# Kernel tuning notes

Hardware: AMD Instinct MI355X
Metric: run time of the kernel (lower is better)

The kernel has to match this reference:

```python
import jax, jax.numpy as jnp
import numpy as np

C = 256
H = 4  # hard-coded head count in SA_Layer reshapes
EPS = 1e-5


def _bn(x, gamma, beta):
    # training-mode BatchNorm1d over (batch, length) per channel; x: [b,c,n]
    m = jnp.mean(x, axis=(0, 2), keepdims=True)
    v = jnp.var(x, axis=(0, 2), keepdims=True)
    return gamma[None, :, None] * (x - m) * jax.lax.rsqrt(v + EPS) + beta[None, :, None]


def _conv1(w, x, b=None):
    # 1x1 Conv1d == per-point matmul; w: [o,c], x: [b,c,n]
    y = jnp.einsum('oc,bcn->bon', w, x)
    return y if b is None else y + b[None, :, None]


def _sa_layer(x, xyz_emb, qk_w, v_w, v_b, t_w, t_b, bn_g, bn_b):
    b, c, n = x.shape
    h = x + xyz_emb                      # [b,c,n]
    q = _conv1(qk_w, h)                  # [b,c,n]  (q and k share weights)
    # quirky reshape: permute to [b,n,c] then view as [b,H,n,c//H]
    x_q = jnp.transpose(q, (0, 2, 1)).reshape(b, H, n, c // H)
    x_k = q.reshape(b, H, c // H, n)     # standard channel head split
    x_v = _conv1(v_w, h, v_b).reshape(b, H, c // H, n)
    energy = jnp.matmul(x_q, x_k)        # [b,H,n,n]
    att = jax.nn.softmax(energy, axis=-1)
    att = jax.nn.softmax(att, axis=-2)   # dual softmax
    x_r = jnp.matmul(x_v, att).reshape(b, c, n)
    x_r = jax.nn.relu(_bn(_conv1(t_w, x - x_r, t_b), bn_g, bn_b))
    return x + x_r


def setup_inputs() -> dict:
    key = jax.random.key(0)
    ks = jax.random.split(key, 16)
    B, N = 4, 2048
    s = 1.0 / np.sqrt(C)
    inp = {
        'x': jax.random.normal(ks[0], (B, C, N), jnp.float32),
        'xyz': jax.random.normal(ks[1], (B, N, 3), jnp.float32),
        'conv1_w': jax.random.normal(ks[2], (C, C), jnp.float32) * s,
        'pos_w': jax.random.normal(ks[3], (C, 3), jnp.float32) * 0.5,
        'pos_b': jax.random.normal(ks[4], (C,), jnp.float32) * 0.02,
        'bn1_g': jnp.ones((C,), jnp.float32),
        'bn1_b': jnp.zeros((C,), jnp.float32),
        'qk_w': jax.random.normal(ks[5], (4, C, C), jnp.float32) * s,
        'v_w': jax.random.normal(ks[6], (4, C, C), jnp.float32) * s,
        'v_b': jax.random.normal(ks[7], (4, C), jnp.float32) * 0.02,
        't_w': jax.random.normal(ks[8], (4, C, C), jnp.float32) * s,
        't_b': jax.random.normal(ks[9], (4, C), jnp.float32) * 0.02,
        'bn_g': jnp.ones((4, C), jnp.float32),
        'bn_b': jnp.zeros((4, C), jnp.float32),
    }
    return inp


def reference(x, xyz, conv1_w, pos_w, pos_b, bn1_g, bn1_b,
              qk_w, v_w, v_b, t_w, t_b, bn_g, bn_b):
    # xyz: [B,N,3] -> permute -> pos_xyz (1x1 conv)
    xyz_emb = jnp.einsum('oi,bni->bon', pos_w, xyz) + pos_b[None, :, None]  # [b,C,n]
    h = jax.nn.relu(_bn(_conv1(conv1_w, x), bn1_g, bn1_b))
    outs = []
    for i in range(4):
        h = _sa_layer(h, xyz_emb, qk_w[i], v_w[i], v_b[i],
                      t_w[i], t_b[i], bn_g[i], bn_b[i])
        outs.append(h)
    return jnp.concatenate(outs, axis=1)  # [b, 4*C, n]
```

## Files before the change

### kernel.cpp

```cpp
#include <hip/hip_runtime.h>
#include <math.h>

#define Bsz 4
#define Cch 256
#define Npt 2048
#define Hh  4
#define NL  4
#define BN_CNT (Bsz * Npt)
#define EPSV 1e-5f
#define NROW (16 * Npt)
#define L2E 1.44269504f

typedef _Float16 f16x8 __attribute__((ext_vector_type(8)));
typedef _Float16 f16x4 __attribute__((ext_vector_type(4)));
typedef float    f32x4 __attribute__((ext_vector_type(4)));

__device__ __forceinline__ float fexp2(float x) { return __builtin_amdgcn_exp2f(x); }

__device__ __forceinline__ void gld16(const _Float16* g, _Float16* l) {
    __builtin_amdgcn_global_load_lds(
        (const __attribute__((address_space(1))) unsigned int*)g,
        (__attribute__((address_space(3))) unsigned int*)l, 16, 0, 0);
}

__global__ void k_xyz_emb(const float* __restrict__ xyz, const float* __restrict__ pw,
                          const float* __restrict__ pb, float* __restrict__ emb) {
    int idx = blockIdx.x * 256 + threadIdx.x;
    int n = idx & (Npt - 1);
    int c = (idx >> 11) & (Cch - 1);
    int b = idx >> 19;
    const float* xz = xyz + (b * Npt + n) * 3;
    emb[idx] = pw[c * 3 + 0] * xz[0] + pw[c * 3 + 1] * xz[1] + pw[c * 3 + 2] * xz[2] + pb[c];
}

__global__ void k_castw(const float* __restrict__ c1w, const float* __restrict__ qkw,
                        const float* __restrict__ vw, const float* __restrict__ tw,
                        _Float16* __restrict__ o, float* __restrict__ bnacc) {
    int i = blockIdx.x * 256 + threadIdx.x;
    if (i < 5 * 512) bnacc[i] = 0.f;
    const float* src; int off;
    if (i < 65536)            { src = c1w; off = i; }
    else if (i < 327680)      { src = qkw; off = i - 65536; }
    else if (i < 589824)      { src = vw;  off = i - 327680; }
    else                      { src = tw;  off = i - 589824; }
    o[i] = (_Float16)src[off];
}

__global__ __launch_bounds__(256) void k_fuse_t(const float* __restrict__ in,
        _Float16* __restrict__ XT) {
    __shared__ _Float16 Tt[64][72];
    const int b = blockIdx.z, c0 = blockIdx.y * 64, n0 = blockIdx.x * 64;
    const int t = threadIdx.x;
    const int cl = t >> 2, ns = (t & 3) * 16;
    const float* ip = in + ((size_t)(b * Cch + c0 + cl) * Npt) + n0 + ns;
    #pragma unroll
    for (int g = 0; g < 4; ++g) {
        float4 v = *(const float4*)(ip + g * 4);
        Tt[ns + g * 4 + 0][cl] = (_Float16)v.x;
        Tt[ns + g * 4 + 1][cl] = (_Float16)v.y;
        Tt[ns + g * 4 + 2][cl] = (_Float16)v.z;
        Tt[ns + g * 4 + 3][cl] = (_Float16)v.w;
    }
    __syncthreads();
    int nl = t >> 2, cs = (t & 3) * 16;
    _Float16* op = XT + ((size_t)(b * Npt + n0 + nl) * Cch) + c0 + cs;
    #pragma unroll
    for (int g = 0; g < 4; ++g)
        *(f16x4*)(op + g * 4) = *(f16x4*)&Tt[nl][cs + g * 4];
}

__global__ __launch_bounds__(256) void k_gemm_mfma(const _Float16* __restrict__ Wb,
        const _Float16* __restrict__ XT, const float* __restrict__ bias,
        float* __restrict__ Yf, float* __restrict__ bnacc) {
    __shared__ float EpF[64][68];
    const int b = blockIdx.z, o0 = blockIdx.y * 64, n0 = blockIdx.x * 64;
    const int tid = threadIdx.x, w = tid >> 6, quad = (tid >> 4) & 3, tx = tid & 15;
    const _Float16* Arow = Wb + (o0 + w * 16 + tx) * Cch + quad * 8;
    const _Float16* Brow = XT + ((size_t)(b * Npt + n0 + tx) * Cch) + quad * 8;
    f32x4 acc[4];
    #pragma unroll
    for (int s = 0; s < 4; ++s) acc[s] = (f32x4){0.f, 0.f, 0.f, 0.f};
    for (int k0 = 0; k0 < Cch; k0 += 32) {
        f16x8 a = *(const f16x8*)(Arow + k0);
        #pragma unroll
        for (int s = 0; s < 4; ++s) {
            f16x8 bb = *(const f16x8*)(Brow + s * 16 * Cch + k0);
            acc[s] = __builtin_amdgcn_mfma_f32_16x16x32_f16(a, bb, acc[s], 0, 0, 0);
        }
    }
    float bv[4];
    {
        int ob = o0 + w * 16 + quad * 4;
        if (bias) { bv[0] = bias[ob]; bv[1] = bias[ob + 1]; bv[2] = bias[ob + 2]; bv[3] = bias[ob + 3]; }
        else bv[0] = bv[1] = bv[2] = bv[3] = 0.f;
    }
    #pragma unroll
    for (int s = 0; s < 4; ++s) {
        int ol = w * 16 + quad * 4, nl = s * 16 + tx;
        EpF[ol + 0][nl] = acc[s][0] + bv[0];
        EpF[ol + 1][nl] = acc[s][1] + bv[1];
        EpF[ol + 2][nl] = acc[s][2] + bv[2];
        EpF[ol + 3][nl] = acc[s][3] + bv[3];
    }
    __syncthreads();
    int row = tid >> 2, seg = (tid & 3) * 16;
    float* yp = Yf + ((size_t)(b * Cch + o0 + row) * Npt) + n0 + seg;
    float s1 = 0.f, s2 = 0.f;
    #pragma unroll
    for (int g = 0; g < 4; ++g) {
        float4 v = *(float4*)&EpF[row][seg + g * 4];
        *(float4*)(yp + g * 4) = v;
        s1 += v.x + v.y + v.z + v.w;
        s2 += v.x * v.x + v.y * v.y + v.z * v.z + v.w * v.w;
    }
    s1 += __shfl_xor(s1, 1); s2 += __shfl_xor(s2, 1);
    s1 += __shfl_xor(s1, 2); s2 += __shfl_xor(s2, 2);
    if ((tid & 3) == 0) {
        atomicAdd(&bnacc[o0 + row], s1);
        atomicAdd(&bnacc[256 + o0 + row], s2);
    }
}

__global__ __launch_bounds__(256) void k_gemm_qkv(const _Float16* __restrict__ Wqk,
        const _Float16* __restrict__ Wv, const _Float16* __restrict__ XT,
        const float* __restrict__ vbias, _Float16* __restrict__ Vb,
        _Float16* __restrict__ Qg, _Float16* __restrict__ Kt) {
    __shared__ _Float16 EpB[64][72];
    const int b = blockIdx.z, y = blockIdx.y, n0 = blockIdx.x * 64;
    const int isV = (y >= 4);
    const int o0 = (isV ? (y - 4) : y) * 64;
    const _Float16* Wb = isV ? Wv : Wqk;
    const int tid = threadIdx.x, w = tid >> 6, quad = (tid >> 4) & 3, tx = tid & 15;
    const _Float16* Arow = Wb + (o0 + w * 16 + tx) * Cch + quad * 8;
    const _Float16* Brow = XT + ((size_t)(b * Npt + n0 + tx) * Cch) + quad * 8;
    f32x4 acc[4];
    #pragma unroll
    for (int s = 0; s < 4; ++s) acc[s] = (f32x4){0.f, 0.f, 0.f, 0.f};
    for (int k0 = 0; k0 < Cch; k0 += 32) {
        f16x8 a = *(const f16x8*)(Arow + k0);
        #pragma unroll
        for (int s = 0; s < 4; ++s) {
            f16x8 bb = *(const f16x8*)(Brow + s * 16 * Cch + k0);
            acc[s] = __builtin_amdgcn_mfma_f32_16x16x32_f16(a, bb, acc[s], 0, 0, 0);
        }
    }
    if (!isV) {
        const int cch = (w << 1) + (quad >> 1);
        const int hof = (quad & 1) * 4;
        #pragma unroll
        for (int s = 0; s < 4; ++s) {
            int ng = n0 + s * 16 + tx;
            f16x4 pk;
            pk[0] = (_Float16)acc[s][0]; pk[1] = (_Float16)acc[s][1];
            pk[2] = (_Float16)acc[s][2]; pk[3] = (_Float16)acc[s][3];
            int rK = ng & 63, jt = ng >> 6;
            size_t ka = ((size_t)((b * Hh + (o0 >> 6)) * 32 + jt) << 12)
                      + rK * 64 + ((cch ^ (rK & 7)) * 8) + hof;
            *(f16x4*)&Kt[ka] = pk;
            int iQ = ((ng & 511) << 2) + (o0 >> 6);
            int rQ = iQ & 63, it = iQ >> 6;
            size_t qa = ((size_t)((b * Hh + (ng >> 9)) * 32 + it) << 12)
                      + rQ * 64 + ((cch ^ (rQ & 7)) * 8) + hof;
            *(f16x4*)&Qg[qa] = pk;
        }
        return;
    }
    float bv[4];
    {
        int ob = o0 + w * 16 + quad * 4;
        bv[0] = vbias[ob]; bv[1] = vbias[ob + 1]; bv[2] = vbias[ob + 2]; bv[3] = vbias[ob + 3];
    }
    #pragma unroll
    for (int s = 0; s < 4; ++s) {
        int ol = w * 16 + quad * 4, nl = s * 16 + tx;
        EpB[ol + 0][nl] = (_Float16)(acc[s][0] + bv[0]);
        EpB[ol + 1][nl] = (_Float16)(acc[s][1] + bv[1]);
        EpB[ol + 2][nl] = (_Float16)(acc[s][2] + bv[2]);
        EpB[ol + 3][nl] = (_Float16)(acc[s][3] + bv[3]);
    }
    __syncthreads();
    int row = tid >> 2, seg = (tid & 3) * 16;
    _Float16* yp = Vb + ((size_t)(b * Cch + o0 + row) * Npt) + n0 + seg;
    #pragma unroll
    for (int g = 0; g < 4; ++g)
        *(f16x4*)(yp + g * 4) = *(f16x4*)&EpB[row][seg + g * 4];
}

__global__ __launch_bounds__(256) void k_attn_A(const _Float16* __restrict__ Qg,
        const _Float16* __restrict__ Kt, float* __restrict__ mP, float* __restrict__ lP) {
    __shared__ _Float16 Ksh[2][4096];
    const int flat = blockIdx.x;
    const int bh = (flat & 7) * 2 + ((flat >> 3) & 1);
    const int rest = flat >> 4;
    const int i0 = (rest & 15) * 128;
    const int jc = rest >> 4;
    const int tid = threadIdx.x, w = tid >> 6, q = (tid >> 4) & 3, tx = tid & 15;
    const int lane = tid & 63;
    const int sx = tx & 7;
    f16x8 qa[2][2];
    #pragma unroll
    for (int g = 0; g < 2; ++g) {
        const _Float16* Qtile = Qg + ((size_t)(bh * 32 + ((i0 + g * 64) >> 6)) << 12);
        int r = w * 16 + tx;
        qa[g][0] = *(const f16x8*)(Qtile + r * 64 + (q ^ sx) * 8);
        qa[g][1] = *(const f16x8*)(Qtile + r * 64 + ((q + 4) ^ sx) * 8);
    }
    const _Float16* Kbase = Kt + ((size_t)(bh * 32) << 12);
    const int jt0 = jc * 8;
    {
        const _Float16* g = Kbase + ((size_t)jt0 << 12) + (w * 2) * 512 + lane * 8;
        gld16(g,       &Ksh[0][(w * 2 + 0) * 512]);
        gld16(g + 512, &Ksh[0][(w * 2 + 1) * 512]);
    }
    __syncthreads();
    float m2[2][4], l[2][4];
    #pragma unroll
    for (int g = 0; g < 2; ++g)
        #pragma unroll
        for (int r = 0; r < 4; ++r) { m2[g][r] = -1e30f; l[g][r] = 0.f; }
    for (int t = 0; t < 8; ++t) {
        if (t < 7) {
            const _Float16* g = Kbase + ((size_t)(jt0 + t + 1) << 12) + (w * 2) * 512 + lane * 8;
            gld16(g,       &Ksh[(t + 1) & 1][(w * 2 + 0) * 512]);
            gld16(g + 512, &Ksh[(t + 1) & 1][(w * 2 + 1) * 512]);
        }
        const _Float16* kbuf = Ksh[t & 1];
        f32x4 e[2][4];
        #pragma unroll
        for (int s = 0; s < 4; ++s) {
            int r = s * 16 + tx;
            f16x8 kb0 = *(const f16x8*)(kbuf + r * 64 + (q ^ sx) * 8);
            f16x8 kb1 = *(const f16x8*)(kbuf + r * 64 + ((q + 4) ^ sx) * 8);
            #pragma unroll
            for (int g = 0; g < 2; ++g) {
                f32x4 z = (f32x4){0.f, 0.f, 0.f, 0.f};
                z = __builtin_amdgcn_mfma_f32_16x16x32_f16(qa[g][0], kb0, z, 0, 0, 0);
                e[g][s] = __builtin_amdgcn_mfma_f32_16x16x32_f16(qa[g][1], kb1, z, 0, 0, 0);
            }
        }
        #pragma unroll
        for (int g = 0; g < 2; ++g)
            #pragma unroll
            for (int r = 0; r < 4; ++r) {
                float e0 = e[g][0][r] * L2E, e1 = e[g][1][r] * L2E;
                float e2 = e[g][2][r] * L2E, e3 = e[g][3][r] * L2E;
                float lm = fmaxf(fmaxf(e0, e1), fmaxf(e2, e3));
                float nm = fmaxf(m2[g][r], lm);
                l[g][r] = l[g][r] * fexp2(m2[g][r] - nm)
                        + fexp2(e0 - nm) + fexp2(e1 - nm) + fexp2(e2 - nm) + fexp2(e3 - nm);
                m2[g][r] = nm;
            }
        __syncthreads();
    }
    #pragma unroll
    for (int g = 0; g < 2; ++g)
        #pragma unroll
        for (int r = 0; r < 4; ++r) {
            float mm = m2[g][r], ll = l[g][r];
            #pragma unroll
            for (int off = 1; off < 16; off <<= 1) {
                float om = __shfl_xor(mm, off), ol = __shfl_xor(ll, off);
                float nm = fmaxf(mm, om);
                ll = ll * fexp2(mm - nm) + ol * fexp2(om - nm);
                mm = nm;
            }
            if (tx == 0) {
                int idx = bh * Npt + i0 + g * 64 + w * 16 + q * 4 + r;
                mP[jc * NROW + idx] = mm;
                lP[jc * NROW + idx] = ll;
            }
        }
}

__global__ __launch_bounds__(256) void k_attn_B(const _Float16* __restrict__ Qg,
        const _Float16* __restrict__ Kt, const _Float16* __restrict__ Vb,
        const float* __restrict__ mP, const float* __restrict__ lP,
        const float* __restrict__ h, _Float16* __restrict__ XT) {
    __shared__ _Float16 AtT[4][4096];
    __shared__ float mlm[Npt];
    __shared__ float mll[Npt];
    __shared__ float Ssh[4][64];
    __shared__ float rsv[64];
    __shared__ _Float16 Tt[64][72];
    const int flat = blockIdx.x;
    const int bh = (flat & 7) * 2 + ((flat >> 3) & 1);
    const int j0 = (flat >> 4) * 64;
    const int b = bh >> 2, hd = bh & 3;
    const int tid = threadIdx.x, w = tid >> 6, q = (tid >> 4) & 3, tx = tid & 15;
    const int sx = tx & 7;
    {
        const int ib = tid * 8;
        #pragma unroll
        for (int e = 0; e < 2; ++e) {
            int ii = ib + e * 4;
            int idx = bh * Npt + ii;
            float4 m0 = *(const float4*)&mP[idx];
            float4 m1 = *(const float4*)&mP[NROW + idx];
            float4 m2 = *(const float4*)&mP[2 * NROW + idx];
            float4 m3 = *(const float4*)&mP[3 * NROW + idx];
            float4 l0 = *(const float4*)&lP[idx];
            float4 l1 = *(const float4*)&lP[NROW + idx];
            float4 l2 = *(const float4*)&lP[2 * NROW + idx];
            float4 l3 = *(const float4*)&lP[3 * NROW + idx];
            #pragma unroll
            for (int k = 0; k < 4; ++k) {
                float a0 = ((const float*)&m0)[k], a1 = ((const float*)&m1)[k];
                float a2 = ((const float*)&m2)[k], a3 = ((const float*)&m3)[k];
                float mm = fmaxf(fmaxf(a0, a1), fmaxf(a2, a3));
                float ll = ((const float*)&l0)[k] * fexp2(a0 - mm)
                         + ((const float*)&l1)[k] * fexp2(a1 - mm)
                         + ((const float*)&l2)[k] * fexp2(a2 - mm)
                         + ((const float*)&l3)[k] * fexp2(a3 - mm);
                mlm[ii + k] = mm;
                mll[ii + k] = L2E / ll;
            }
        }
    }
    __syncthreads();
    f16x8 kb[4][2];
    const _Float16* Ktile = Kt + ((size_t)(bh * 32 + (j0 >> 6)) << 12);
    #pragma unroll
    for (int nt = 0; nt < 4; ++nt) {
        int r = nt * 16 + tx;
        kb[nt][0] = *(const f16x8*)(Ktile + r * 64 + (q ^ sx) * 8);
        kb[nt][1] = *(const f16x8*)(Ktile + r * 64 + ((q + 4) ^ sx) * 8);
    }
    f32x4 Tacc[4][4];
    #pragma unroll
    for (int mt = 0; mt < 4; ++mt)
        #pragma unroll
        for (int nt = 0; nt < 4; ++nt) Tacc[mt][nt] = (f32x4){0.f, 0.f, 0.f, 0.f};
    float scS[4] = {0.f, 0.f, 0.f, 0.f};
    _Float16* myAt = AtT[w];
    const _Float16* vbase = Vb + (size_t)(b * Cch + hd * 64) * Npt;
    for (int it = 0; it < 8; ++it) {
        const int i0 = w * 512 + it * 64;
        const _Float16* Qtile = Qg + ((size_t)(bh * 32 + (i0 >> 6)) << 12);
        #pragma unroll
        for (int mt = 0; mt < 4; ++mt) {
            int r = mt * 16 + tx;
            f16x8 qa0 = *(const f16x8*)(Qtile + r * 64 + (q ^ sx) * 8);
            f16x8 qa1 = *(const f16x8*)(Qtile + r * 64 + ((q + 4) ^ sx) * 8);
            float4 m2v = *(const float4*)&mlm[i0 + mt * 16 + q * 4];
            float4 liv = *(const float4*)&mll[i0 + mt * 16 + q * 4];
            #pragma unroll
            for (int nt = 0; nt < 4; ++nt) {
                f32x4 z = (f32x4){0.f, 0.f, 0.f, 0.f};
                z = __builtin_amdgcn_mfma_f32_16x16x32_f16(qa0, kb[nt][0], z, 0, 0, 0);
                z = __builtin_amdgcn_mfma_f32_16x16x32_f16(qa1, kb[nt][1], z, 0, 0, 0);
                float a0 = fexp2(fexp2(__builtin_fmaf(z[0], L2E, -m2v.x)) * liv.x);
                float a1 = fexp2(fexp2(__builtin_fmaf(z[1], L2E, -m2v.y)) * liv.y);
                float a2 = fexp2(fexp2(__builtin_fmaf(z[2], L2E, -m2v.z)) * liv.z);
                float a3 = fexp2(fexp2(__builtin_fmaf(z[3], L2E, -m2v.w)) * liv.w);
                scS[nt] += a0 + a1 + a2 + a3;
                f16x4 pk;
                pk[0] = (_Float16)a0; pk[1] = (_Float16)a1;
                pk[2] = (_Float16)a2; pk[3] = (_Float16)a3;
                *(f16x4*)&myAt[(nt * 16 + tx) * 64 + ((2 * mt + (q >> 1)) ^ sx) * 8 + (q & 1) * 4] = pk;
            }
        }
        f16x8 pb[4][2], va[4][2];
        #pragma unroll
        for (int nt = 0; nt < 4; ++nt) {
            int r = nt * 16 + tx;
            pb[nt][0] = *(const f16x8*)&myAt[r * 64 + (q ^ sx) * 8];
            pb[nt][1] = *(const f16x8*)&myAt[r * 64 + ((q + 4) ^ sx) * 8];
        }
        #pragma unroll
        for (int mt = 0; mt < 4; ++mt) {
            const _Float16* vp = vbase + (size_t)(mt * 16 + tx) * Npt + i0 + q * 8;
            va[mt][0] = *(const f16x8*)(vp);
            va[mt][1] = *(const f16x8*)(vp + 32);
        }
        #pragma unroll
        for (int mt = 0; mt < 4; ++mt)
            #pragma unroll
            for (int nt = 0; nt < 4; ++nt) {
                Tacc[mt][nt] = __builtin_amdgcn_mfma_f32_16x16x32_f16(va[mt][0], pb[nt][0], Tacc[mt][nt], 0, 0, 0);
                Tacc[mt][nt] = __builtin_amdgcn_mfma_f32_16x16x32_f16(va[mt][1], pb[nt][1], Tacc[mt][nt], 0, 0, 0);
            }
    }
    #pragma unroll
    for (int mt = 0; mt < 4; ++mt)
        #pragma unroll
        for (int nt = 0; nt < 4; ++nt) {
            f16x4 pk;
            pk[0] = (_Float16)Tacc[mt][nt][0];
            pk[1] = (_Float16)Tacc[mt][nt][1];
            pk[2] = (_Float16)Tacc[mt][nt][2];
            pk[3] = (_Float16)Tacc[mt][nt][3];
            *(f16x4*)&myAt[(nt * 16 + tx) * 64 + mt * 16 + q * 4] = pk;
        }
    #pragma unroll
    for (int nt = 0; nt < 4; ++nt) {
        float s = scS[nt];
        s += __shfl_xor(s, 16);
        s += __shfl_xor(s, 32);
        if (q == 0) Ssh[w][nt * 16 + tx] = s;
    }
    __syncthreads();
    if (tid < 64)
        rsv[tid] = 1.f / (Ssh[0][tid] + Ssh[1][tid] + Ssh[2][tid] + Ssh[3][tid]);
    __syncthreads();
    {
        const int cl = tid >> 2, ns = (tid & 3) * 16;
        const float* hp = h + ((size_t)(b * Cch + hd * 64 + cl) * Npt) + j0 + ns;
        #pragma unroll
        for (int g = 0; g < 4; ++g) {
            float4 hv = *(const float4*)(hp + g * 4);
            #pragma unroll
            for (int k = 0; k < 4; ++k) {
                int jl = ns + g * 4 + k;
                float tv = (float)AtT[0][jl * 64 + cl] + (float)AtT[1][jl * 64 + cl]
                         + (float)AtT[2][jl * 64 + cl] + (float)AtT[3][jl * 64 + cl];
                float hvk = ((const float*)&hv)[k];
                Tt[jl][cl] = (_Float16)(hvk - tv * rsv[jl]);
            }
        }
    }
    __syncthreads();
    {
        int nl = tid >> 2, cs = (tid & 3) * 16;
        _Float16* op = XT + ((size_t)(b * Npt + j0 + nl) * Cch) + hd * 64 + cs;
        #pragma unroll
        for (int g = 0; g < 4; ++g)
            *(f16x4*)(op + g * 4) = *(f16x4*)&Tt[nl][cs + g * 4];
    }
}

__global__ __launch_bounds__(256) void k_bn_fuse(const float* __restrict__ t,
        const float* __restrict__ bnacc,
        const float* __restrict__ g, const float* __restrict__ bt,
        const float* __restrict__ emb, const float* __restrict__ resid,
        float* __restrict__ hout, float* __restrict__ out, _Float16* __restrict__ XT,
        int layer) {
    __shared__ _Float16 Tt[64][72];
    const int b = blockIdx.z, c0 = blockIdx.y * 64, n0 = blockIdx.x * 64;
    const int tt = threadIdx.x;
    const int cl = tt >> 2, ns = (tt & 3) * 16;
    const int c = c0 + cl;
    const float mn = bnacc[c] * (1.f / BN_CNT);
    const float var = bnacc[256 + c] * (1.f / BN_CNT) - mn * mn;
    const float is = rsqrtf(var + EPSV);
    const float gg = g[c], bb = bt[c];
    const size_t rowoff = ((size_t)(b * Cch + c) * Npt) + n0 + ns;
    const float* tp = t + rowoff;
    const float* ep = emb + rowoff;
    const float* rp = resid ? resid + rowoff : nullptr;
    float* hp = hout + rowoff;
    float* op = out ? out + (size_t)b * (NL * Cch * Npt) + (size_t)(layer * Cch + c) * Npt + n0 + ns
                    : nullptr;
    #pragma unroll
    for (int gi = 0; gi < 4; ++gi) {
        float4 v = *(const float4*)(tp + gi * 4);
        float4 y;
        y.x = fmaxf(gg * (v.x - mn) * is + bb, 0.f);
        y.y = fmaxf(gg * (v.y - mn) * is + bb, 0.f);
        y.z = fmaxf(gg * (v.z - mn) * is + bb, 0.f);
        y.w = fmaxf(gg * (v.w - mn) * is + bb, 0.f);
        if (rp) {
            float4 r = *(const float4*)(rp + gi * 4);
            y.x += r.x; y.y += r.y; y.z += r.z; y.w += r.w;
        }
        *(float4*)(hp + gi * 4) = y;
        if (op) *(float4*)(op + gi * 4) = y;
        float4 e = *(const float4*)(ep + gi * 4);
        Tt[ns + gi * 4 + 0][cl] = (_Float16)(y.x + e.x);
        Tt[ns + gi * 4 + 1][cl] = (_Float16)(y.y + e.y);
        Tt[ns + gi * 4 + 2][cl] = (_Float16)(y.z + e.z);
        Tt[ns + gi * 4 + 3][cl] = (_Float16)(y.w + e.w);
    }
    __syncthreads();
    int nl = tt >> 2, cs = (tt & 3) * 16;
    _Float16* xp = XT + ((size_t)(b * Npt + n0 + nl) * Cch) + c0 + cs;
    #pragma unroll
    for (int gi = 0; gi < 4; ++gi)
        *(f16x4*)(xp + gi * 4) = *(f16x4*)&Tt[nl][cs + gi * 4];
}

extern "C" void kernel_launch(void* const* d_in, const int* in_sizes, int n_in,
                              void* d_out, int out_size, void* d_ws, size_t ws_size,
                              hipStream_t stream) {
    (void)in_sizes; (void)n_in; (void)out_size; (void)ws_size;
    const float* x    = (const float*)d_in[0];
    const float* xyz  = (const float*)d_in[1];
    const float* c1w  = (const float*)d_in[2];
    const float* posw = (const float*)d_in[3];
    const float* posb = (const float*)d_in[4];
    const float* bn1g = (const float*)d_in[5];
    const float* bn1b = (const float*)d_in[6];
    const float* qkw  = (const float*)d_in[7];
    const float* vw   = (const float*)d_in[8];
    const float* vb   = (const float*)d_in[9];
    const float* tw   = (const float*)d_in[10];
    const float* tb   = (const float*)d_in[11];
    const float* bng  = (const float*)d_in[12];
    const float* bnb  = (const float*)d_in[13];
    float* out = (float*)d_out;

    const size_t NE = (size_t)Bsz * Cch * Npt;
    char* W = (char*)d_ws;
    float* emb   = (float*)W;                 W += NE * 4;
    float* h     = (float*)W;                 W += NE * 4;
    float* vbuf  = (float*)W;                 W += NE * 4;
    _Float16* XT = (_Float16*)W;              W += NE * 2;
    _Float16* Qg = (_Float16*)W;              W += NE * 2;
    _Float16* Kt = (_Float16*)W;              W += NE * 2;
    _Float16* Vb = (_Float16*)W;              W += NE * 2;
    _Float16* wbf = (_Float16*)W;             W += 851968 * 2;
    float* mP    = (float*)W;                 W += 4 * NROW * 4;
    float* lP    = (float*)W;                 W += 4 * NROW * 4;
    float* bnacc = (float*)W;                 W += 5 * 512 * 4;

    dim3 blk(256);
    dim3 g4(Npt / 64, Cch / 64, Bsz);
    dim3 gQKV(Npt / 64, 8, Bsz);
    int ew = (int)(NE / 256);

    k_castw<<<3328, blk, 0, stream>>>(c1w, qkw, vw, tw, wbf, bnacc);
    k_xyz_emb<<<ew, blk, 0, stream>>>(xyz, posw, posb, emb);

    k_fuse_t<<<g4, blk, 0, stream>>>(x, XT);
    k_gemm_mfma<<<g4, blk, 0, stream>>>(wbf, XT, nullptr, vbuf, bnacc);
    k_bn_fuse<<<g4, blk, 0, stream>>>(vbuf, bnacc, bn1g, bn1b, emb, nullptr,
                                      h, nullptr, XT, 0);

    for (int L = 0; L < NL; ++L) {
        const _Float16* qkL = wbf + 65536 + (size_t)L * 65536;
        const _Float16* vL  = wbf + 327680 + (size_t)L * 65536;
        const _Float16* tL  = wbf + 589824 + (size_t)L * 65536;
        float* accL = bnacc + (1 + L) * 512;
        k_gemm_qkv<<<gQKV, blk, 0, stream>>>(qkL, vL, XT, vb + L * Cch, Vb, Qg, Kt);
        k_attn_A<<<1024, blk, 0, stream>>>(Qg, Kt, mP, lP);
        k_attn_B<<<512, blk, 0, stream>>>(Qg, Kt, Vb, mP, lP, h, XT);
        k_gemm_mfma<<<g4, blk, 0, stream>>>(tL, XT, tb + L * Cch, vbuf, accL);
        k_bn_fuse<<<g4, blk, 0, stream>>>(vbuf, accL, bng + L * Cch, bnb + L * Cch,
                                          emb, h, h, out, XT, L);
    }
}
```

Measured before the change: 603.4 us.

## Halve attn_B column tile to 32 and double grid, rewrite epilogue

Shrinks each k_attn_B block from 64 to 32 output columns (j), doubling the grid from 512 to 1024 blocks and halving per-block LDS and accumulator registers. The aim is better occupancy and more parallelism across CUs. The cost is that every block recomputes the full Q·K exponentials over all 2048 rows and reloads V for only half as many columns, which doubles that redundant work. The epilogue now writes the transposed accumulator with a swizzled layout and reads it back directly, with no separate Tt staging buffer or extra barrier.

```diff
diff --git a/kernel.cpp b/kernel.cpp
--- a/kernel.cpp
+++ b/kernel.cpp
@@ -276,15 +276,14 @@
         const _Float16* __restrict__ Kt, const _Float16* __restrict__ Vb,
         const float* __restrict__ mP, const float* __restrict__ lP,
         const float* __restrict__ h, _Float16* __restrict__ XT) {
-    __shared__ _Float16 AtT[4][4096];
+    __shared__ _Float16 AtT[4][2048];
     __shared__ float mlm[Npt];
     __shared__ float mll[Npt];
-    __shared__ float Ssh[4][64];
-    __shared__ float rsv[64];
-    __shared__ _Float16 Tt[64][72];
+    __shared__ float Ssh[4][32];
+    __shared__ float rsv[32];
     const int flat = blockIdx.x;
     const int bh = (flat & 7) * 2 + ((flat >> 3) & 1);
-    const int j0 = (flat >> 4) * 64;
+    const int j0 = (flat >> 4) * 32;
     const int b = bh >> 2, hd = bh & 3;
     const int tid = threadIdx.x, w = tid >> 6, q = (tid >> 4) & 3, tx = tid & 15;
     const int sx = tx & 7;
@@ -317,20 +316,21 @@
         }
     }
     __syncthreads();
-    f16x8 kb[4][2];
+    f16x8 kb[2][2];
     const _Float16* Ktile = Kt + ((size_t)(bh * 32 + (j0 >> 6)) << 12);
-    #pragma unroll
-    for (int nt = 0; nt < 4; ++nt) {
-        int r = nt * 16 + tx;
+    const int jb = j0 & 32;
+    #pragma unroll
+    for (int nt = 0; nt < 2; ++nt) {
+        int r = jb + nt * 16 + tx;
         kb[nt][0] = *(const f16x8*)(Ktile + r * 64 + (q ^ sx) * 8);
         kb[nt][1] = *(const f16x8*)(Ktile + r * 64 + ((q + 4) ^ sx) * 8);
     }
-    f32x4 Tacc[4][4];
+    f32x4 Tacc[4][2];
     #pragma unroll
     for (int mt = 0; mt < 4; ++mt)
         #pragma unroll
-        for (int nt = 0; nt < 4; ++nt) Tacc[mt][nt] = (f32x4){0.f, 0.f, 0.f, 0.f};
-    float scS[4] = {0.f, 0.f, 0.f, 0.f};
+        for (int nt = 0; nt < 2; ++nt) Tacc[mt][nt] = (f32x4){0.f, 0.f, 0.f, 0.f};
+    float scS[2] = {0.f, 0.f};
     _Float16* myAt = AtT[w];
     const _Float16* vbase = Vb + (size_t)(b * Cch + hd * 64) * Npt;
     for (int it = 0; it < 8; ++it) {
@@ -344,7 +344,7 @@
             float4 m2v = *(const float4*)&mlm[i0 + mt * 16 + q * 4];
             float4 liv = *(const float4*)&mll[i0 + mt * 16 + q * 4];
             #pragma unroll
-            for (int nt = 0; nt < 4; ++nt) {
+            for (int nt = 0; nt < 2; ++nt) {
                 f32x4 z = (f32x4){0.f, 0.f, 0.f, 0.f};
                 z = __builtin_amdgcn_mfma_f32_16x16x32_f16(qa0, kb[nt][0], z, 0, 0, 0);
                 z = __builtin_amdgcn_mfma_f32_16x16x32_f16(qa1, kb[nt][1], z, 0, 0, 0);
@@ -359,9 +359,9 @@
                 *(f16x4*)&myAt[(nt * 16 + tx) * 64 + ((2 * mt + (q >> 1)) ^ sx) * 8 + (q & 1) * 4] = pk;
             }
         }
-        f16x8 pb[4][2], va[4][2];
-        #pragma unroll
-        for (int nt = 0; nt < 4; ++nt) {
+        f16x8 pb[2][2], va[4][2];
+        #pragma unroll
+        for (int nt = 0; nt < 2; ++nt) {
             int r = nt * 16 + tx;
             pb[nt][0] = *(const f16x8*)&myAt[r * 64 + (q ^ sx) * 8];
             pb[nt][1] = *(const f16x8*)&myAt[r * 64 + ((q + 4) ^ sx) * 8];
@@ -375,7 +375,7 @@
         #pragma unroll
         for (int mt = 0; mt < 4; ++mt)
             #pragma unroll
-            for (int nt = 0; nt < 4; ++nt) {
+            for (int nt = 0; nt < 2; ++nt) {
                 Tacc[mt][nt] = __builtin_amdgcn_mfma_f32_16x16x32_f16(va[mt][0], pb[nt][0], Tacc[mt][nt], 0, 0, 0);
                 Tacc[mt][nt] = __builtin_amdgcn_mfma_f32_16x16x32_f16(va[mt][1], pb[nt][1], Tacc[mt][nt], 0, 0, 0);
             }
@@ -383,48 +383,42 @@
     #pragma unroll
     for (int mt = 0; mt < 4; ++mt)
         #pragma unroll
-        for (int nt = 0; nt < 4; ++nt) {
+        for (int nt = 0; nt < 2; ++nt) {
             f16x4 pk;
             pk[0] = (_Float16)Tacc[mt][nt][0];
             pk[1] = (_Float16)Tacc[mt][nt][1];
             pk[2] = (_Float16)Tacc[mt][nt][2];
             pk[3] = (_Float16)Tacc[mt][nt][3];
-            *(f16x4*)&myAt[(nt * 16 + tx) * 64 + mt * 16 + q * 4] = pk;
-        }
-    #pragma unroll
-    for (int nt = 0; nt < 4; ++nt) {
+            *(f16x4*)&myAt[(nt * 16 + tx) * 64 + ((2 * mt + (q >> 1)) ^ sx) * 8 + (q & 1) * 4] = pk;
+        }
+    #pragma unroll
+    for (int nt = 0; nt < 2; ++nt) {
         float s = scS[nt];
         s += __shfl_xor(s, 16);
         s += __shfl_xor(s, 32);
         if (q == 0) Ssh[w][nt * 16 + tx] = s;
     }
     __syncthreads();
-    if (tid < 64)
+    if (tid < 32)
         rsv[tid] = 1.f / (Ssh[0][tid] + Ssh[1][tid] + Ssh[2][tid] + Ssh[3][tid]);
     __syncthreads();
     {
-        const int cl = tid >> 2, ns = (tid & 3) * 16;
-        const float* hp = h + ((size_t)(b * Cch + hd * 64 + cl) * Npt) + j0 + ns;
-        #pragma unroll
-        for (int g = 0; g < 4; ++g) {
-            float4 hv = *(const float4*)(hp + g * 4);
-            #pragma unroll
-            for (int k = 0; k < 4; ++k) {
-                int jl = ns + g * 4 + k;
-                float tv = (float)AtT[0][jl * 64 + cl] + (float)AtT[1][jl * 64 + cl]
-                         + (float)AtT[2][jl * 64 + cl] + (float)AtT[3][jl * 64 + cl];
-                float hvk = ((const float*)&hv)[k];
-                Tt[jl][cl] = (_Float16)(hvk - tv * rsv[jl]);
-            }
-        }
-    }
-    __syncthreads();
-    {
-        int nl = tid >> 2, cs = (tid & 3) * 16;
-        _Float16* op = XT + ((size_t)(b * Npt + j0 + nl) * Cch) + hd * 64 + cs;
-        #pragma unroll
-        for (int g = 0; g < 4; ++g)
-            *(f16x4*)(op + g * 4) = *(f16x4*)&Tt[nl][cs + g * 4];
+        const int jl = tid >> 3, half = tid & 7;
+        const int slot = ((half ^ (jl & 7)) * 8);
+        const int base = jl * 64 + slot;
+        f16x8 t0 = *(const f16x8*)&AtT[0][base];
+        f16x8 t1 = *(const f16x8*)&AtT[1][base];
+        f16x8 t2 = *(const f16x8*)&AtT[2][base];
+        f16x8 t3 = *(const f16x8*)&AtT[3][base];
+        const float rs = rsv[jl];
+        const float* hp = h + ((size_t)(b * Cch + hd * 64 + half * 8) * Npt) + j0 + jl;
+        f16x8 u;
+        #pragma unroll
+        for (int e = 0; e < 8; ++e) {
+            float tv = (float)t0[e] + (float)t1[e] + (float)t2[e] + (float)t3[e];
+            u[e] = (_Float16)(hp[(size_t)e * Npt] - tv * rs);
+        }
+        *(f16x8*)(XT + ((size_t)(b * Npt + j0 + jl) * Cch) + hd * 64 + half * 8) = u;
     }
 }
 
@@ -532,7 +526,7 @@
         float* accL = bnacc + (1 + L) * 512;
         k_gemm_qkv<<<gQKV, blk, 0, stream>>>(qkL, vL, XT, vb + L * Cch, Vb, Qg, Kt);
         k_attn_A<<<1024, blk, 0, stream>>>(Qg, Kt, mP, lP);
-        k_attn_B<<<512, blk, 0, stream>>>(Qg, Kt, Vb, mP, lP, h, XT);
+        k_attn_B<<<1024, blk, 0, stream>>>(Qg, Kt, Vb, mP, lP, h, XT);
         k_gemm_mfma<<<g4, blk, 0, stream>>>(tL, XT, tb + L * Cch, vbuf, accL);
         k_bn_fuse<<<g4, blk, 0, stream>>>(vbuf, accL, bng + L * Cch, bnb + L * Cch,
                                           emb, h, h, out, XT, L);
```

After: 634.2 us. 5.1% more time.

## Restructure attention-B to 512 threads, register-resident P tiles and permuted V layout

Applied to the files above, without the earlier changes.

The second attention kernel now runs with 8 waves per block, each covering 256 query rows instead of 512. K is staged into LDS with a direct global-to-LDS load instead of being held in registers. The softmax probabilities are passed straight from the QK MFMA outputs into the PV MFMA as register operands, which removes the per-wave LDS round-trip. To make that work, the V store in the QKV GEMM permutes its column layout so V matches the interleaved P fragment order. The cross-wave reduction of the PV partials is done in two halves to fit LDS, trading extra barriers and shared memory for more parallelism and less LDS traffic.

```diff
diff --git a/kernel.cpp b/kernel.cpp
--- a/kernel.cpp
+++ b/kernel.cpp
@@ -180,10 +180,12 @@
     }
     __syncthreads();
     int row = tid >> 2, seg = (tid & 3) * 16;
-    _Float16* yp = Vb + ((size_t)(b * Cch + o0 + row) * Npt) + n0 + seg;
+    const int m = tid & 3;
+    const int pbase = (m >> 1) * 32 + (m & 1) * 4;
+    _Float16* yp = Vb + ((size_t)(b * Cch + o0 + row) * Npt) + n0 + pbase;
     #pragma unroll
     for (int g = 0; g < 4; ++g)
-        *(f16x4*)(yp + g * 4) = *(f16x4*)&EpB[row][seg + g * 4];
+        *(f16x4*)(yp + g * 8) = *(f16x4*)&EpB[row][seg + g * 4];
 }
 
 __global__ __launch_bounds__(256) void k_attn_A(const _Float16* __restrict__ Qg,
@@ -272,125 +274,99 @@
         }
 }
 
-__global__ __launch_bounds__(256) void k_attn_B(const _Float16* __restrict__ Qg,
+__global__ __launch_bounds__(512, 4) void k_attn_B(const _Float16* __restrict__ Qg,
         const _Float16* __restrict__ Kt, const _Float16* __restrict__ Vb,
         const float* __restrict__ mP, const float* __restrict__ lP,
         const float* __restrict__ h, _Float16* __restrict__ XT) {
-    __shared__ _Float16 AtT[4][4096];
+    __shared__ _Float16 Ksh[4096];
     __shared__ float mlm[Npt];
     __shared__ float mll[Npt];
-    __shared__ float Ssh[4][64];
+    __shared__ float Ssh[8][64];
     __shared__ float rsv[64];
-    __shared__ _Float16 Tt[64][72];
+    __shared__ _Float16 TS[8][2048];
     const int flat = blockIdx.x;
     const int bh = (flat & 7) * 2 + ((flat >> 3) & 1);
     const int j0 = (flat >> 4) * 64;
     const int b = bh >> 2, hd = bh & 3;
     const int tid = threadIdx.x, w = tid >> 6, q = (tid >> 4) & 3, tx = tid & 15;
-    const int sx = tx & 7;
+    const int lane = tid & 63, sx = tx & 7;
     {
-        const int ib = tid * 8;
-        #pragma unroll
-        for (int e = 0; e < 2; ++e) {
-            int ii = ib + e * 4;
-            int idx = bh * Npt + ii;
-            float4 m0 = *(const float4*)&mP[idx];
-            float4 m1 = *(const float4*)&mP[NROW + idx];
-            float4 m2 = *(const float4*)&mP[2 * NROW + idx];
-            float4 m3 = *(const float4*)&mP[3 * NROW + idx];
-            float4 l0 = *(const float4*)&lP[idx];
-            float4 l1 = *(const float4*)&lP[NROW + idx];
-            float4 l2 = *(const float4*)&lP[2 * NROW + idx];
-            float4 l3 = *(const float4*)&lP[3 * NROW + idx];
-            #pragma unroll
-            for (int k = 0; k < 4; ++k) {
-                float a0 = ((const float*)&m0)[k], a1 = ((const float*)&m1)[k];
-                float a2 = ((const float*)&m2)[k], a3 = ((const float*)&m3)[k];
-                float mm = fmaxf(fmaxf(a0, a1), fmaxf(a2, a3));
-                float ll = ((const float*)&l0)[k] * fexp2(a0 - mm)
-                         + ((const float*)&l1)[k] * fexp2(a1 - mm)
-                         + ((const float*)&l2)[k] * fexp2(a2 - mm)
-                         + ((const float*)&l3)[k] * fexp2(a3 - mm);
-                mlm[ii + k] = mm;
-                mll[ii + k] = L2E / ll;
-            }
-        }
-    }
-    __syncthreads();
-    f16x8 kb[4][2];
-    const _Float16* Ktile = Kt + ((size_t)(bh * 32 + (j0 >> 6)) << 12);
-    #pragma unroll
-    for (int nt = 0; nt < 4; ++nt) {
-        int r = nt * 16 + tx;
-        kb[nt][0] = *(const f16x8*)(Ktile + r * 64 + (q ^ sx) * 8);
-        kb[nt][1] = *(const f16x8*)(Ktile + r * 64 + ((q + 4) ^ sx) * 8);
-    }
+        const int ii = tid * 4;
+        const int idx = bh * Npt + ii;
+        float4 m0 = *(const float4*)&mP[idx];
+        float4 m1 = *(const float4*)&mP[NROW + idx];
+        float4 m2 = *(const float4*)&mP[2 * NROW + idx];
+        float4 m3 = *(const float4*)&mP[3 * NROW + idx];
+        float4 l0 = *(const float4*)&lP[idx];
+        float4 l1 = *(const float4*)&lP[NROW + idx];
+        float4 l2 = *(const float4*)&lP[2 * NROW + idx];
+        float4 l3 = *(const float4*)&lP[3 * NROW + idx];
+        #pragma unroll
+        for (int k = 0; k < 4; ++k) {
+            float a0 = ((const float*)&m0)[k], a1 = ((const float*)&m1)[k];
+            float a2 = ((const float*)&m2)[k], a3 = ((const float*)&m3)[k];
+            float mm = fmaxf(fmaxf(a0, a1), fmaxf(a2, a3));
+            float ll = ((const float*)&l0)[k] * fexp2(a0 - mm)
+                     + ((const float*)&l1)[k] * fexp2(a1 - mm)
+                     + ((const float*)&l2)[k] * fexp2(a2 - mm)
+                     + ((const float*)&l3)[k] * fexp2(a3 - mm);
+            mlm[ii + k] = mm;
+            mll[ii + k] = L2E / ll;
+        }
+    }
+    gld16(Kt + (((size_t)(bh * 32 + (j0 >> 6))) << 12) + w * 512 + lane * 8, &Ksh[w * 512]);
+    __syncthreads();
     f32x4 Tacc[4][4];
     #pragma unroll
     for (int mt = 0; mt < 4; ++mt)
         #pragma unroll
         for (int nt = 0; nt < 4; ++nt) Tacc[mt][nt] = (f32x4){0.f, 0.f, 0.f, 0.f};
     float scS[4] = {0.f, 0.f, 0.f, 0.f};
-    _Float16* myAt = AtT[w];
     const _Float16* vbase = Vb + (size_t)(b * Cch + hd * 64) * Npt;
-    for (int it = 0; it < 8; ++it) {
-        const int i0 = w * 512 + it * 64;
+    for (int it = 0; it < 4; ++it) {
+        const int i0 = w * 256 + it * 64;
         const _Float16* Qtile = Qg + ((size_t)(bh * 32 + (i0 >> 6)) << 12);
         #pragma unroll
-        for (int mt = 0; mt < 4; ++mt) {
-            int r = mt * 16 + tx;
-            f16x8 qa0 = *(const f16x8*)(Qtile + r * 64 + (q ^ sx) * 8);
-            f16x8 qa1 = *(const f16x8*)(Qtile + r * 64 + ((q + 4) ^ sx) * 8);
-            float4 m2v = *(const float4*)&mlm[i0 + mt * 16 + q * 4];
-            float4 liv = *(const float4*)&mll[i0 + mt * 16 + q * 4];
-            #pragma unroll
-            for (int nt = 0; nt < 4; ++nt) {
-                f32x4 z = (f32x4){0.f, 0.f, 0.f, 0.f};
-                z = __builtin_amdgcn_mfma_f32_16x16x32_f16(qa0, kb[nt][0], z, 0, 0, 0);
-                z = __builtin_amdgcn_mfma_f32_16x16x32_f16(qa1, kb[nt][1], z, 0, 0, 0);
-                float a0 = fexp2(fexp2(__builtin_fmaf(z[0], L2E, -m2v.x)) * liv.x);
-                float a1 = fexp2(fexp2(__builtin_fmaf(z[1], L2E, -m2v.y)) * liv.y);
-                float a2 = fexp2(fexp2(__builtin_fmaf(z[2], L2E, -m2v.z)) * liv.z);
-                float a3 = fexp2(fexp2(__builtin_fmaf(z[3], L2E, -m2v.w)) * liv.w);
-                scS[nt] += a0 + a1 + a2 + a3;
-                f16x4 pk;
-                pk[0] = (_Float16)a0; pk[1] = (_Float16)a1;
-                pk[2] = (_Float16)a2; pk[3] = (_Float16)a3;
-                *(f16x4*)&myAt[(nt * 16 + tx) * 64 + ((2 * mt + (q >> 1)) ^ sx) * 8 + (q & 1) * 4] = pk;
+        for (int pp = 0; pp < 2; ++pp) {
+            f16x4 pk[2][4];
+            #pragma unroll
+            for (int mt2 = 0; mt2 < 2; ++mt2) {
+                const int mt = pp * 2 + mt2;
+                const int r = mt * 16 + tx;
+                f16x8 qa0 = *(const f16x8*)(Qtile + r * 64 + (q ^ sx) * 8);
+                f16x8 qa1 = *(const f16x8*)(Qtile + r * 64 + ((q + 4) ^ sx) * 8);
+                float4 m2v = *(const float4*)&mlm[i0 + mt * 16 + q * 4];
+                float4 liv = *(const float4*)&mll[i0 + mt * 16 + q * 4];
+                #pragma unroll
+                for (int nt = 0; nt < 4; ++nt) {
+                    const int rk = nt * 16 + tx;
+                    f16x8 kb0 = *(const f16x8*)&Ksh[rk * 64 + (q ^ sx) * 8];
+                    f16x8 kb1 = *(const f16x8*)&Ksh[rk * 64 + ((q + 4) ^ sx) * 8];
+                    f32x4 z = (f32x4){0.f, 0.f, 0.f, 0.f};
+                    z = __builtin_amdgcn_mfma_f32_16x16x32_f16(qa0, kb0, z, 0, 0, 0);
+                    z = __builtin_amdgcn_mfma_f32_16x16x32_f16(qa1, kb1, z, 0, 0, 0);
+                    float a0 = fexp2(fexp2(__builtin_fmaf(z[0], L2E, -m2v.x)) * liv.x);
+                    float a1 = fexp2(fexp2(__builtin_fmaf(z[1], L2E, -m2v.y)) * liv.y);
+                    float a2 = fexp2(fexp2(__builtin_fmaf(z[2], L2E, -m2v.z)) * liv.z);
+                    float a3 = fexp2(fexp2(__builtin_fmaf(z[3], L2E, -m2v.w)) * liv.w);
+                    scS[nt] += a0 + a1 + a2 + a3;
+                    f16x4 pkk;
+                    pkk[0] = (_Float16)a0; pkk[1] = (_Float16)a1;
+                    pkk[2] = (_Float16)a2; pkk[3] = (_Float16)a3;
+                    pk[mt2][nt] = pkk;
+                }
             }
-        }
-        f16x8 pb[4][2], va[4][2];
-        #pragma unroll
-        for (int nt = 0; nt < 4; ++nt) {
-            int r = nt * 16 + tx;
-            pb[nt][0] = *(const f16x8*)&myAt[r * 64 + (q ^ sx) * 8];
-            pb[nt][1] = *(const f16x8*)&myAt[r * 64 + ((q + 4) ^ sx) * 8];
-        }
-        #pragma unroll
-        for (int mt = 0; mt < 4; ++mt) {
-            const _Float16* vp = vbase + (size_t)(mt * 16 + tx) * Npt + i0 + q * 8;
-            va[mt][0] = *(const f16x8*)(vp);
-            va[mt][1] = *(const f16x8*)(vp + 32);
-        }
-        #pragma unroll
-        for (int mt = 0; mt < 4; ++mt)
-            #pragma unroll
-            for (int nt = 0; nt < 4; ++nt) {
-                Tacc[mt][nt] = __builtin_amdgcn_mfma_f32_16x16x32_f16(va[mt][0], pb[nt][0], Tacc[mt][nt], 0, 0, 0);
-                Tacc[mt][nt] = __builtin_amdgcn_mfma_f32_16x16x32_f16(va[mt][1], pb[nt][1], Tacc[mt][nt], 0, 0, 0);
+            #pragma unroll
+            for (int mtd = 0; mtd < 4; ++mtd) {
+                f16x8 va = *(const f16x8*)(vbase + (size_t)(mtd * 16 + tx) * Npt + i0 + pp * 32 + q * 8);
+                #pragma unroll
+                for (int nt = 0; nt < 4; ++nt) {
+                    f16x8 pb = __builtin_shufflevector(pk[0][nt], pk[1][nt], 0, 1, 2, 3, 4, 5, 6, 7);
+                    Tacc[mtd][nt] = __builtin_amdgcn_mfma_f32_16x16x32_f16(va, pb, Tacc[mtd][nt], 0, 0, 0);
+                }
             }
-    }
-    #pragma unroll
-    for (int mt = 0; mt < 4; ++mt)
-        #pragma unroll
-        for (int nt = 0; nt < 4; ++nt) {
-            f16x4 pk;
-            pk[0] = (_Float16)Tacc[mt][nt][0];
-            pk[1] = (_Float16)Tacc[mt][nt][1];
-            pk[2] = (_Float16)Tacc[mt][nt][2];
-            pk[3] = (_Float16)Tacc[mt][nt][3];
-            *(f16x4*)&myAt[(nt * 16 + tx) * 64 + mt * 16 + q * 4] = pk;
-        }
+        }
+    }
     #pragma unroll
     for (int nt = 0; nt < 4; ++nt) {
         float s = scS[nt];
@@ -398,33 +374,75 @@
         s += __shfl_xor(s, 32);
         if (q == 0) Ssh[w][nt * 16 + tx] = s;
     }
+    #pragma unroll
+    for (int mt = 0; mt < 4; ++mt)
+        #pragma unroll
+        for (int nt = 0; nt < 2; ++nt) {
+            f16x4 pkk;
+            pkk[0] = (_Float16)Tacc[mt][nt][0];
+            pkk[1] = (_Float16)Tacc[mt][nt][1];
+            pkk[2] = (_Float16)Tacc[mt][nt][2];
+            pkk[3] = (_Float16)Tacc[mt][nt][3];
+            *(f16x4*)&TS[w][(nt * 16 + tx) * 64 + ((2 * mt + (q >> 1)) ^ sx) * 8 + (q & 1) * 4] = pkk;
+        }
     __syncthreads();
     if (tid < 64)
-        rsv[tid] = 1.f / (Ssh[0][tid] + Ssh[1][tid] + Ssh[2][tid] + Ssh[3][tid]);
-    __syncthreads();
-    {
-        const int cl = tid >> 2, ns = (tid & 3) * 16;
-        const float* hp = h + ((size_t)(b * Cch + hd * 64 + cl) * Npt) + j0 + ns;
-        #pragma unroll
-        for (int g = 0; g < 4; ++g) {
-            float4 hv = *(const float4*)(hp + g * 4);
-            #pragma unroll
-            for (int k = 0; k < 4; ++k) {
-                int jl = ns + g * 4 + k;
-                float tv = (float)AtT[0][jl * 64 + cl] + (float)AtT[1][jl * 64 + cl]
-                         + (float)AtT[2][jl * 64 + cl] + (float)AtT[3][jl * 64 + cl];
-                float hvk = ((const float*)&hv)[k];
-                Tt[jl][cl] = (_Float16)(hvk - tv * rsv[jl]);
-            }
-        }
-    }
-    __syncthreads();
-    {
-        int nl = tid >> 2, cs = (tid & 3) * 16;
-        _Float16* op = XT + ((size_t)(b * Npt + j0 + nl) * Cch) + hd * 64 + cs;
-        #pragma unroll
-        for (int g = 0; g < 4; ++g)
-            *(f16x4*)(op + g * 4) = *(f16x4*)&Tt[nl][cs + g * 4];
+        rsv[tid] = 1.f / (Ssh[0][tid] + Ssh[1][tid] + Ssh[2][tid] + Ssh[3][tid]
+                        + Ssh[4][tid] + Ssh[5][tid] + Ssh[6][tid] + Ssh[7][tid]);
+    const int jl = (tid >> 3) & 31, d8 = tid & 7;
+    const int tsbase = jl * 64 + ((d8 ^ (jl & 7)) * 8);
+    float tsum[8];
+    if (tid < 256) {
+        #pragma unroll
+        for (int e = 0; e < 8; ++e) tsum[e] = 0.f;
+        #pragma unroll
+        for (int wv = 0; wv < 8; ++wv) {
+            f16x8 t = *(const f16x8*)&TS[wv][tsbase];
+            #pragma unroll
+            for (int e = 0; e < 8; ++e) tsum[e] += (float)t[e];
+        }
+    }
+    __syncthreads();
+    if (tid < 256) {
+        const int jg = j0 + jl;
+        const float rs = rsv[jl];
+        const float* hp = h + ((size_t)(b * Cch + hd * 64 + d8 * 8) * Npt) + jg;
+        f16x8 u;
+        #pragma unroll
+        for (int e = 0; e < 8; ++e)
+            u[e] = (_Float16)(hp[(size_t)e * Npt] - tsum[e] * rs);
+        *(f16x8*)(XT + ((size_t)(b * Npt + jg) * Cch) + hd * 64 + d8 * 8) = u;
+    }
+    #pragma unroll
+    for (int mt = 0; mt < 4; ++mt)
+        #pragma unroll
+        for (int nt = 2; nt < 4; ++nt) {
+            f16x4 pkk;
+            pkk[0] = (_Float16)Tacc[mt][nt][0];
+            pkk[1] = (_Float16)Tacc[mt][nt][1];
+            pkk[2] = (_Float16)Tacc[mt][nt][2];
+            pkk[3] = (_Float16)Tacc[mt][nt][3];
+            *(f16x4*)&TS[w][((nt - 2) * 16 + tx) * 64 + ((2 * mt + (q >> 1)) ^ sx) * 8 + (q & 1) * 4] = pkk;
+        }
+    __syncthreads();
+    if (tid < 256) {
+        float t2[8];
+        #pragma unroll
+        for (int e = 0; e < 8; ++e) t2[e] = 0.f;
+        #pragma unroll
+        for (int wv = 0; wv < 8; ++wv) {
+            f16x8 t = *(const f16x8*)&TS[wv][tsbase];
+            #pragma unroll
+            for (int e = 0; e < 8; ++e) t2[e] += (float)t[e];
+        }
+        const int jg = j0 + 32 + jl;
+        const float rs = rsv[32 + jl];
+        const float* hp = h + ((size_t)(b * Cch + hd * 64 + d8 * 8) * Npt) + jg;
+        f16x8 u;
+        #pragma unroll
+        for (int e = 0; e < 8; ++e)
+            u[e] = (_Float16)(hp[(size_t)e * Npt] - t2[e] * rs);
+        *(f16x8*)(XT + ((size_t)(b * Npt + jg) * Cch) + hd * 64 + d8 * 8) = u;
     }
 }
 
@@ -532,7 +550,7 @@
         float* accL = bnacc + (1 + L) * 512;
         k_gemm_qkv<<<gQKV, blk, 0, stream>>>(qkL, vL, XT, vb + L * Cch, Vb, Qg, Kt);
         k_attn_A<<<1024, blk, 0, stream>>>(Qg, Kt, mP, lP);
-        k_attn_B<<<512, blk, 0, stream>>>(Qg, Kt, Vb, mP, lP, h, XT);
+        k_attn_B<<<512, dim3(512), 0, stream>>>(Qg, Kt, Vb, mP, lP, h, XT);
         k_gemm_mfma<<<g4, blk, 0, stream>>>(tL, XT, tb + L * Cch, vbuf, accL);
         k_bn_fuse<<<g4, blk, 0, stream>>>(vbuf, accL, bng + L * Cch, bnb + L * Cch,
                                           emb, h, h, out, XT, L);
```

Result: slower. 1.044 ms (+73.1%).
